# Optimization experiments

Measured on AMD Instinct MI355X. Metric: run time of the kernel, lower is better.

The kernel has to match this reference:

```python
import jax, jax.numpy as jnp
import numpy as np

B, L, D_IN, D, DEPTH, H = 1, 4095, 1536, 768, 4, 12
HD = D // H
FFN = 4 * D
GRID = 128
TILE = 256
SEGMENTS = (1024, 2048, 4096, 8192, 16384)
RATIOS = (1, 2, 4, 8, 16)
EPS = 1e-5
NEG = -1e9


def _sincos_1d(d, pos):
    omega = 1.0 / (10000.0 ** (np.arange(d // 2, dtype=np.float64) / (d / 2.0)))
    out = np.einsum('m,d->md', pos.reshape(-1).astype(np.float64), omega)
    return np.concatenate([np.sin(out), np.cos(out)], axis=1)


def _pos_embed_2d(d, g):
    # MAE-style 2d sincos grid; row index = coords[...,0], col = coords[...,1]
    gw, gh = np.meshgrid(np.arange(g, dtype=np.float64), np.arange(g, dtype=np.float64))
    emb_h = _sincos_1d(d // 2, gw)
    emb_w = _sincos_1d(d // 2, gh)
    pe = np.concatenate([emb_h, emb_w], axis=1)  # [g*g, d]
    return np.concatenate([np.zeros((1, d)), pe], axis=0).astype(np.float32)  # cls row


def setup_inputs() -> dict:
    key = jax.random.key(0)
    ks = jax.random.split(key, 16)
    n = lambda k, sh: 0.02 * jax.random.normal(k, sh, jnp.float32)
    x = jax.random.normal(ks[0], (B, L, D_IN), jnp.float32)
    coords = jax.random.uniform(ks[1], (B, L, 2), jnp.float32, 0.0, float(GRID * TILE))
    return {
        'x': x,
        'coords': coords,
        'pos_embed': jnp.asarray(_pos_embed_2d(D, GRID)),
        'cls_token': n(ks[2], (1, 1, D)),
        'patch_w': n(ks[3], (D_IN, D)),
        'patch_b': jnp.zeros((D,), jnp.float32),
        'ln1_g': jnp.ones((DEPTH, D), jnp.float32),
        'ln1_b': jnp.zeros((DEPTH, D), jnp.float32),
        'wq': n(ks[4], (DEPTH, D, D)), 'bq': jnp.zeros((DEPTH, D), jnp.float32),
        'wk': n(ks[5], (DEPTH, D, D)), 'bk': jnp.zeros((DEPTH, D), jnp.float32),
        'wv': n(ks[6], (DEPTH, D, D)), 'bv': jnp.zeros((DEPTH, D), jnp.float32),
        'wo': n(ks[7], (DEPTH, D, D)), 'bo': jnp.zeros((DEPTH, D), jnp.float32),
        'ln2_g': jnp.ones((DEPTH, D), jnp.float32),
        'ln2_b': jnp.zeros((DEPTH, D), jnp.float32),
        'w1': n(ks[8], (DEPTH, D, FFN)), 'b1': jnp.zeros((DEPTH, FFN), jnp.float32),
        'w2': n(ks[9], (DEPTH, FFN, D)), 'b2': jnp.zeros((DEPTH, D), jnp.float32),
        'enc_ln_g': jnp.ones((D,), jnp.float32),
        'enc_ln_b': jnp.zeros((D,), jnp.float32),
        'norm_g': jnp.ones((D,), jnp.float32),
        'norm_b': jnp.zeros((D,), jnp.float32),
    }


def _ln(t, g, b):
    m = t.mean(-1, keepdims=True)
    v = ((t - m) ** 2).mean(-1, keepdims=True)
    return (t - m) * jax.lax.rsqrt(v + EPS) * g + b


def _branch(q, k, v, w, r):
    # One LongNet dilated branch: segments of length w, per-head dilation r.
    Bq, S, Hh, hd = q.shape
    Lp = ((S + w - 1) // w) * w
    pad = Lp - S
    if pad:
        q = jnp.pad(q, ((0, 0), (0, pad), (0, 0), (0, 0)))
        k = jnp.pad(k, ((0, 0), (0, pad), (0, 0), (0, 0)))
        v = jnp.pad(v, ((0, 0), (0, pad), (0, 0), (0, 0)))
    n = Lp // w
    m = w // r
    # head-dependent offset subsampling (offset = head % r)
    idx = (jnp.arange(Hh) % r)[:, None] + r * jnp.arange(m)[None, :]  # [H, m]

    def seg(t):
        t = t.reshape(Bq, n, w, Hh, hd).transpose(0, 1, 3, 2, 4)  # [B,n,H,w,hd]
        return jnp.take_along_axis(t, idx[None, None, :, :, None], axis=3)  # [B,n,H,m,hd]

    qs, ks, vs = seg(q), seg(k), seg(v)
    valid = (jnp.arange(n)[:, None, None] * w + idx[None]) < S  # [n,H,m] key validity
    s = jnp.einsum('bnhqd,bnhkd->bnhqk', qs, ks)
    s = jnp.where(valid[None, :, :, None, :], s, NEG)
    lse_s = jax.scipy.special.logsumexp(s, axis=-1)              # [B,n,H,m]
    o_s = jnp.einsum('bnhqk,bnhkd->bnhqd', jax.nn.softmax(s, axis=-1), vs)
    hix = jnp.arange(Hh)[:, None]
    out = jnp.zeros((Bq, n, Hh, w, hd), q.dtype).at[:, :, hix, idx].set(o_s)
    lse = jnp.full((Bq, n, Hh, w), NEG, q.dtype).at[:, :, hix, idx].set(lse_s)
    out = out.transpose(0, 1, 3, 2, 4).reshape(Bq, Lp, Hh, hd)[:, :S]
    lse = lse.transpose(0, 1, 3, 2).reshape(Bq, Lp, Hh)[:, :S]
    return out, lse


def _forward(x, coords, pos_embed, cls_token, patch_w, patch_b, ln1_g, ln1_b,
             wq, bq, wk, bk, wv, bv, wo, bo, ln2_g, ln2_b, w1, b1, w2, b2,
             enc_ln_g, enc_ln_b, norm_g, norm_b):
    h = x @ patch_w + patch_b  # PatchEmbed (norm_layer=None -> Identity)
    c = jnp.floor(coords / TILE)
    pos = (c[..., 0] * GRID + c[..., 1]).astype(jnp.int32) + 1  # [B,L]
    h = h + pos_embed[pos]
    cls = jnp.broadcast_to(cls_token + pos_embed[0], (h.shape[0], 1, D))
    h = jnp.concatenate([cls, h], axis=1)  # [B, S, D], S = L+1
    S = h.shape[1]

    def layer(hcur, p):
        g1, bb1, wq_, bq_, wk_, bk_, wv_, bv_, wo_, bo_, g2, bb2, wf1, bf1, wf2, bf2 = p
        t = _ln(hcur, g1, bb1)
        q = (t @ wq_ + bq_).reshape(B, S, H, HD) * (HD ** -0.5)
        k = (t @ wk_ + bk_).reshape(B, S, H, HD)
        v = (t @ wv_ + bv_).reshape(B, S, H, HD)
        outs, lses = [], []
        for w_, r_ in zip(SEGMENTS, RATIOS):
            o, l = _branch(q, k, v, w_, r_)
            outs.append(o)
            lses.append(l)
        # LongNet combine: branches weighted by their softmax denominators
        wts = jax.nn.softmax(jnp.stack(lses), axis=0)  # [nb,B,S,H]
        attn = (wts[..., None] * jnp.stack(outs)).sum(0).reshape(B, S, D)
        hcur = hcur + attn @ wo_ + bo_
        t = _ln(hcur, g2, bb2)
        hcur = hcur + jax.nn.gelu(t @ wf1 + bf1) @ wf2 + bf2
        return hcur, None

    h, _ = jax.lax.scan(layer, h, (ln1_g, ln1_b, wq, bq, wk, bk, wv, bv,
                                   wo, bo, ln2_g, ln2_b, w1, b1, w2, b2))
    h = _ln(h, enc_ln_g, enc_ln_b)  # encoder final LN (normalize_before)
    h = _ln(h, norm_g, norm_b)      # module self.norm
    return h[:, 0]                  # cls token (global_pool=False)


def reference(x, coords, pos_embed, cls_token, patch_w, patch_b, ln1_g, ln1_b,
              wq, bq, wk, bk, wv, bv, wo, bo, ln2_g, ln2_b, w1, b1, w2, b2,
              enc_ln_g, enc_ln_b, norm_g, norm_b):
    return _forward(x, coords, pos_embed, cls_token, patch_w, patch_b, ln1_g, ln1_b,
                    wq, bq, wk, bk, wv, bv, wo, bo, ln2_g, ln2_b, w1, b1, w2, b2,
                    enc_ln_g, enc_ln_b, norm_g, norm_b)
```

## Files before the change

### kernel.cpp

```cpp
#include <hip/hip_runtime.h>
#include <hip/hip_bf16.h>
#include <math.h>
#include <stdint.h>

#define S_LEN 4096
#define L_LEN 4095
#define DIN   1536
#define DM    768
#define NHEAD 12
#define HDIM  64
#define FFND  3072
#define EPS   1e-5f

typedef unsigned short u16;
typedef unsigned int   u32;
typedef short short8 __attribute__((ext_vector_type(8)));
typedef float f32x4 __attribute__((ext_vector_type(4)));
typedef float f32x16 __attribute__((ext_vector_type(16)));
typedef int i32x2 __attribute__((ext_vector_type(2)));

__device__ __forceinline__ u16 f2b(float f) {
    union { float f; u32 u; } x; x.f = f;
    u32 r = (x.u + 0x7FFF + ((x.u >> 16) & 1)) >> 16;
    return (u16)r;
}
__device__ __forceinline__ float b2f(u16 v) {
    union { u32 u; float f; } x; x.u = ((u32)v) << 16;
    return x.f;
}
__device__ __forceinline__ float gelu_tanh(float x) {
    float x3 = x * x * x;
    return 0.5f * x * (1.f + tanhf(0.7978845608f * (x + 0.044715f * x3)));
}
__device__ __forceinline__ float block_reduce_sum(float v, float* sbuf) {
#pragma unroll
    for (int o = 32; o > 0; o >>= 1) v += __shfl_down(v, o, 64);
    __syncthreads();
    if ((threadIdx.x & 63) == 0) sbuf[threadIdx.x >> 6] = v;
    __syncthreads();
    return sbuf[0] + sbuf[1] + sbuf[2] + sbuf[3];
}
__device__ __forceinline__ void gload16(const void* g, void* l) {
    __builtin_amdgcn_global_load_lds((const __attribute__((address_space(1))) void*)g,
                                     (__attribute__((address_space(3))) void*)l,
                                     16, 0, 0);
}
__device__ __forceinline__ void lds_barrier() {
    asm volatile("s_waitcnt lgkmcnt(0)" ::: "memory");
    __builtin_amdgcn_s_barrier();
    __builtin_amdgcn_sched_barrier(0);
}

template <int BM, int BN>
__device__ __forceinline__ void gemm_bt(
    const u16* __restrict__ A, const u16* __restrict__ Bt,
    const float* __restrict__ bias, const float* __restrict__ res,
    float* __restrict__ outf, u16* __restrict__ outb,
    int M, int N, int K, float scale, int dogelu, int bx, int by)
{
    constexpr int MI = BM / 32;
    constexpr int NI = BN / 32;
    constexpr int AI = BM / 32;
    constexpr int BI = BN / 32;
    __shared__ u16 As[BM * 64];
    __shared__ u16 Bs[BN * 64];
    const int tid = threadIdx.x, wv = tid >> 6, l = tid & 63;
    const int bm = by * BM, bn = bx * BN;
    const int wm = wv >> 1, wn = wv & 1;

    f32x4 acc[MI][NI];
#pragma unroll
    for (int i = 0; i < MI; ++i)
#pragma unroll
        for (int j = 0; j < NI; ++j) acc[i][j] = (f32x4){0.f, 0.f, 0.f, 0.f};

    for (int k0 = 0; k0 < K; k0 += 64) {
#pragma unroll
        for (int i = 0; i < AI; ++i) {
            int row = (wv * AI + i) * 8 + (l >> 3);
            int col = ((l & 7) ^ (row & 7)) * 8;
            int grow = bm + row; if (grow > M - 1) grow = M - 1;
            gload16(A + (size_t)grow * K + k0 + col, &As[(wv * AI + i) * 512]);
        }
#pragma unroll
        for (int i = 0; i < BI; ++i) {
            int row = (wv * BI + i) * 8 + (l >> 3);
            int col = ((l & 7) ^ (row & 7)) * 8;
            gload16(Bt + (size_t)(bn + row) * K + k0 + col, &Bs[(wv * BI + i) * 512]);
        }
        __syncthreads();
#pragma unroll
        for (int kc = 0; kc < 2; ++kc) {
            short8 a[MI], b[NI];
#pragma unroll
            for (int mi = 0; mi < MI; ++mi) {
                int row = wm * (BM / 2) + mi * 16 + (l & 15);
                int off = ((l >> 4) * 16 + kc * 64) ^ ((row & 7) << 4);
                a[mi] = *(const short8*)&As[(row * 128 + off) >> 1];
            }
#pragma unroll
            for (int ni = 0; ni < NI; ++ni) {
                int row = wn * (BN / 2) + ni * 16 + (l & 15);
                int off = ((l >> 4) * 16 + kc * 64) ^ ((row & 7) << 4);
                b[ni] = *(const short8*)&Bs[(row * 128 + off) >> 1];
            }
#pragma unroll
            for (int mi = 0; mi < MI; ++mi)
#pragma unroll
                for (int ni = 0; ni < NI; ++ni)
                    acc[mi][ni] = __builtin_amdgcn_mfma_f32_16x16x32_bf16(
                        a[mi], b[ni], acc[mi][ni], 0, 0, 0);
        }
        __syncthreads();
    }
#pragma unroll
    for (int mi = 0; mi < MI; ++mi) {
#pragma unroll
        for (int rg = 0; rg < 4; ++rg) {
            int row = bm + wm * (BM / 2) + mi * 16 + (l >> 4) * 4 + rg;
            if (row >= M) continue;
#pragma unroll
            for (int ni = 0; ni < NI; ++ni) {
                int col = bn + wn * (BN / 2) + ni * 16 + (l & 15);
                float v = (acc[mi][ni][rg] + bias[col]) * scale;
                if (dogelu) v = gelu_tanh(v);
                if (res) v += res[(size_t)row * N + col];
                if (outf) outf[(size_t)row * N + col] = v;
                if (outb) outb[(size_t)row * N + col] = f2b(v);
            }
        }
    }
}

__global__ __launch_bounds__(256) void gemm128_kernel(
    const u16* __restrict__ A, const u16* __restrict__ Bt,
    const float* __restrict__ bias, const float* __restrict__ res,
    float* __restrict__ outf, u16* __restrict__ outb,
    int M, int N, int K, float scale, int dogelu)
{
    gemm_bt<128, 128>(A, Bt, bias, res, outf, outb, M, N, K, scale, dogelu,
                      blockIdx.x, blockIdx.y);
}
__global__ __launch_bounds__(256) void gemm12864_kernel(
    const u16* __restrict__ A, const u16* __restrict__ Bt,
    const float* __restrict__ bias, const float* __restrict__ res,
    float* __restrict__ outf, u16* __restrict__ outb,
    int M, int N, int K, float scale, int dogelu)
{
    gemm_bt<128, 64>(A, Bt, bias, res, outf, outb, M, N, K, scale, dogelu,
                     blockIdx.x, blockIdx.y);
}
__global__ __launch_bounds__(256) void qkv_kernel(
    const u16* __restrict__ t,
    const u16* __restrict__ wqT, const u16* __restrict__ wkT, const u16* __restrict__ wvT,
    const float* __restrict__ bq, const float* __restrict__ bk, const float* __restrict__ bv,
    u16* __restrict__ q, u16* __restrict__ k, u16* __restrict__ v)
{
    int z = blockIdx.z;
    const u16* B = (z == 0) ? wqT : (z == 1) ? wkT : wvT;
    const float* bias = (z == 0) ? bq : (z == 1) ? bk : bv;
    u16* C = (z == 0) ? q : (z == 1) ? k : v;
    float scale = (z == 0) ? 0.125f * 1.4426950408889634f : 1.0f;
    gemm_bt<128, 128>(t, B, bias, nullptr, nullptr, C, S_LEN, DM, DM, scale, 0,
                      blockIdx.x, blockIdx.y);
}

__global__ __launch_bounds__(256) void transpose_cvt(
    const float* __restrict__ s0, const float* __restrict__ s1,
    const float* __restrict__ s2, const float* __restrict__ s3,
    u16* __restrict__ dst, int K, int N)
{
    int z = blockIdx.z;
    const float* src = (z == 0) ? s0 : (z == 1) ? s1 : (z == 2) ? s2 : s3;
    u16* d = dst + (size_t)z * K * N;
    __shared__ float tile[64][65];
    const int t = threadIdx.x;
    const int tk = blockIdx.y * 64, tn = blockIdx.x * 64;
    const int r0 = t >> 4, c0 = (t & 15) * 4;
#pragma unroll
    for (int i = 0; i < 4; ++i) {
        const float* sp = &src[(size_t)(tk + r0 + i * 16) * N + tn + c0];
        tile[r0 + i * 16][c0 + 0] = sp[0];
        tile[r0 + i * 16][c0 + 1] = sp[1];
        tile[r0 + i * 16][c0 + 2] = sp[2];
        tile[r0 + i * 16][c0 + 3] = sp[3];
    }
    __syncthreads();
#pragma unroll
    for (int i = 0; i < 4; ++i) {
        int nr = r0 + i * 16;
        u32 lo = (u32)f2b(tile[c0 + 0][nr]) | ((u32)f2b(tile[c0 + 1][nr]) << 16);
        u32 hi = (u32)f2b(tile[c0 + 2][nr]) | ((u32)f2b(tile[c0 + 3][nr]) << 16);
        *(uint2*)&d[(size_t)(tn + nr) * K + tk + c0] = make_uint2(lo, hi);
    }
}

__global__ __launch_bounds__(256) void prep_weights(
    const float* __restrict__ wq, const float* __restrict__ wk,
    const float* __restrict__ wv, const float* __restrict__ wo,
    const float* __restrict__ w1, const float* __restrict__ w2,
    u16* __restrict__ wbase, int l0)
{
    const size_t DD = (size_t)DM * DM;
    const size_t DF = (size_t)DM * FFND;
    const int layer = l0 + blockIdx.y;
    const size_t lDD = (size_t)layer * DD;
    const size_t lDF = (size_t)layer * DF;
    u16* dstbase = wbase + (size_t)blockIdx.y * (4 * DD + 2 * DF);

    __shared__ float tile[64][65];
    const int id = blockIdx.x;
    const float* src; u16* dst; int K, N, tk64, tn64;
    if (id < 576) {
        int z = id / 144, rm = id % 144;
        src = ((z == 0) ? wq : (z == 1) ? wk : (z == 2) ? wv : wo) + lDD;
        dst = dstbase + (size_t)z * DD;
        K = DM; N = DM; tk64 = rm / 12; tn64 = rm % 12;
    } else if (id < 1152) {
        int rm = id - 576;
        src = w1 + lDF; dst = dstbase + 4 * DD;
        K = DM; N = FFND; tk64 = rm / 48; tn64 = rm % 48;
    } else {
        int rm = id - 1152;
        src = w2 + lDF; dst = dstbase + 4 * DD + DF;
        K = FFND; N = DM; tk64 = rm / 12; tn64 = rm % 12;
    }
    const int t = threadIdx.x;
    const int tk = tk64 * 64, tn = tn64 * 64;
    const int r0 = t >> 4, c0 = (t & 15) * 4;
#pragma unroll
    for (int i = 0; i < 4; ++i) {
        const float* sp = &src[(size_t)(tk + r0 + i * 16) * N + tn + c0];
        tile[r0 + i * 16][c0 + 0] = sp[0];
        tile[r0 + i * 16][c0 + 1] = sp[1];
        tile[r0 + i * 16][c0 + 2] = sp[2];
        tile[r0 + i * 16][c0 + 3] = sp[3];
    }
    __syncthreads();
#pragma unroll
    for (int i = 0; i < 4; ++i) {
        int nr = r0 + i * 16;
        u32 lo = (u32)f2b(tile[c0 + 0][nr]) | ((u32)f2b(tile[c0 + 1][nr]) << 16);
        u32 hi = (u32)f2b(tile[c0 + 2][nr]) | ((u32)f2b(tile[c0 + 3][nr]) << 16);
        *(uint2*)&dst[(size_t)(tn + nr) * K + tk + c0] = make_uint2(lo, hi);
    }
}

__global__ __launch_bounds__(256) void cvt_bf16_kernel(
    const float* __restrict__ x, u16* __restrict__ xb, int n4)
{
    int stride = gridDim.x * 256;
    for (int i = blockIdx.x * 256 + threadIdx.x; i < n4; i += stride) {
        float4 v = ((const float4*)x)[i];
        u32 lo = (u32)f2b(v.x) | ((u32)f2b(v.y) << 16);
        u32 hi = (u32)f2b(v.z) | ((u32)f2b(v.w) << 16);
        ((uint2*)xb)[i] = make_uint2(lo, hi);
    }
}

__global__ __launch_bounds__(192) void ln_kernel(
    const float* __restrict__ in, u16* __restrict__ out,
    const float* __restrict__ g, const float* __restrict__ b)
{
    __shared__ float sA[3], sB[3];
    const int s = blockIdx.x, tid = threadIdx.x;
    float4 x = ((const float4*)(in + (size_t)s * DM))[tid];
    float sum = x.x + x.y + x.z + x.w;
#pragma unroll
    for (int o = 32; o > 0; o >>= 1) sum += __shfl_down(sum, o, 64);
    if ((tid & 63) == 0) sA[tid >> 6] = sum;
    __syncthreads();
    float m = (sA[0] + sA[1] + sA[2]) * (1.f / DM);
    float dx = x.x - m, dy = x.y - m, dz = x.z - m, dw = x.w - m;
    float vs = dx * dx + dy * dy + dz * dz + dw * dw;
#pragma unroll
    for (int o = 32; o > 0; o >>= 1) vs += __shfl_down(vs, o, 64);
    if ((tid & 63) == 0) sB[tid >> 6] = vs;
    __syncthreads();
    float rs = rsqrtf((sB[0] + sB[1] + sB[2]) * (1.f / DM) + EPS);
    float4 gv = ((const float4*)g)[tid];
    float4 bv = ((const float4*)b)[tid];
    u32 lo = (u32)f2b(dx * rs * gv.x + bv.x) | ((u32)f2b(dy * rs * gv.y + bv.y) << 16);
    u32 hi = (u32)f2b(dz * rs * gv.z + bv.z) | ((u32)f2b(dw * rs * gv.w + bv.w) << 16);
    ((uint2*)(out + (size_t)s * DM))[tid] = make_uint2(lo, hi);
}

__global__ __launch_bounds__(256) void posadd_kernel(
    float* __restrict__ h, const float* __restrict__ coords,
    const float* __restrict__ pe, const float* __restrict__ cls)
{
    const int s = blockIdx.x;
    const int tid = threadIdx.x;
    if (s == 0) {
        for (int c = tid; c < DM; c += 256) h[c] = cls[c] + pe[c];
    } else {
        float c0 = floorf(coords[(size_t)(s - 1) * 2 + 0] * (1.f / 256.f));
        float c1 = floorf(coords[(size_t)(s - 1) * 2 + 1] * (1.f / 256.f));
        int pos = (int)(c0 * 128.f + c1) + 1;
        float* hr = h + (size_t)s * DM;
        const float* pr = pe + (size_t)pos * DM;
        for (int c = tid; c < DM; c += 256) hr[c] += pr[c];
    }
}

__global__ __launch_bounds__(256, 4) void attn_kernel(
    const u16* __restrict__ qb, const u16* __restrict__ kbuf, const u16* __restrict__ vb,
    u16* __restrict__ obuf, u16* __restrict__ tp, float* __restrict__ den)
{
    __shared__ u16 Vt[2][64 * 64];

    const int tid = threadIdx.x, wv = tid >> 6, l = tid & 63;
    const int lq = l & 31, lh = l >> 5;
    const int bid = blockIdx.x;
    int b, half = 0, qtile, head, seg = 0;
    if (bid < 768) {
        b = 0; int i = bid; half = i & 1; qtile = (i >> 1) & 7;
        int rest = i >> 4; head = rest % 12; seg = rest / 12;
    } else if (bid < 1152) {
        b = 1; int i = bid - 768; half = i & 1; qtile = (i >> 1) & 7;
        int rest = i >> 4; head = rest % 12; seg = rest / 12;
    } else if (bid < 1344) {
        b = 2; int i = bid - 1152; half = i & 1; qtile = (i >> 1) & 7;
        head = i >> 4;
    } else if (bid < 1392) {
        b = 3; int i = bid - 1344; qtile = i & 3; head = i >> 2;
    } else {
        b = 4; int i = bid - 1392; qtile = i & 1; head = i >> 1;
    }
    const int slot = (b < 3) ? b * 2 + half : 3 + b;
    const int r = 1 << b;
    const int w = 1024 << b;
    const int keyoff = (b < 3) ? half * 512 : 0;
    const int ntiles = (b == 4) ? 4 : 8;
    const size_t base = (size_t)seg * w + (head & (r - 1));
    const int q0 = qtile * 128 + wv * 32;
    const size_t kstep = (size_t)r * DM;

    const size_t sq_l = base + (size_t)r * (q0 + lq);
    const u16* qp = qb + sq_l * DM + head * 64 + lh * 8;
    short8 qf[4];
#pragma unroll
    for (int s = 0; s < 4; ++s) qf[s] = *(const short8*)(qp + s * 16);

    const u16* kp = kbuf + (base + (size_t)r * (keyoff + lq)) * DM + head * 64 + lh * 8;
    const int c = tid & 7, pp = tid >> 3;
    const u16* vsrc = vb + (base + (size_t)r * (keyoff + 2 * pp)) * DM + head * 64 + c * 8;

#define VPACK(dstbuf, A8, B8) do {                                          \
    _Pragma("unroll") for (int j = 0; j < 8; ++j) {                         \
        int i_ = (j + c) & 7; int hd_ = c * 8 + i_;                         \
        u32 val_ = (u32)(u16)(A8)[i_] | ((u32)(u16)(B8)[i_] << 16);         \
        int byte_ = hd_ * 128 + ((pp * 4) ^ (i_ << 4));                     \
        *(u32*)&Vt[dstbuf][byte_ >> 1] = val_; } } while (0)

    f32x16 oacc0 = {0.f,0.f,0.f,0.f,0.f,0.f,0.f,0.f,0.f,0.f,0.f,0.f,0.f,0.f,0.f,0.f};
    f32x16 oacc1 = oacc0;
    float dl = 0.f;

    short8 van = *(const short8*)vsrc;
    short8 vbn = *(const short8*)(vsrc + kstep);
    VPACK(0, van, vbn);
    van = *(const short8*)(vsrc + 64 * kstep);
    vbn = *(const short8*)(vsrc + 65 * kstep);
    short8 kf[8];
#pragma unroll
    for (int s = 0; s < 4; ++s) {
        kf[s]     = *(const short8*)(kp + s * 16);
        kf[4 + s] = *(const short8*)(kp + 32 * kstep + s * 16);
    }
    lds_barrier();

    for (int t = 0; t < ntiles; ++t) {
        const int curb = t & 1;
        f32x16 s0 = {0.f,0.f,0.f,0.f,0.f,0.f,0.f,0.f,0.f,0.f,0.f,0.f,0.f,0.f,0.f,0.f};
        f32x16 s1 = s0;
#pragma unroll
        for (int s = 0; s < 4; ++s)
            s0 = __builtin_amdgcn_mfma_f32_32x32x16_bf16(kf[s], qf[s], s0, 0, 0, 0);
#pragma unroll
        for (int s = 0; s < 4; ++s)
            s1 = __builtin_amdgcn_mfma_f32_32x32x16_bf16(kf[4 + s], qf[s], s1, 0, 0, 0);

        if (t + 1 < ntiles) {
            const u16* kn = kp + (size_t)(t + 1) * 64 * kstep;
#pragma unroll
            for (int s = 0; s < 4; ++s) {
                kf[s]     = *(const short8*)(kn + s * 16);
                kf[4 + s] = *(const short8*)(kn + 32 * kstep + s * 16);
            }
        }

        float ds = 0.f;
#pragma unroll
        for (int i = 0; i < 16; ++i) { s0[i] = exp2f(s0[i]); ds += s0[i]; }
#pragma unroll
        for (int i = 0; i < 16; ++i) { s1[i] = exp2f(s1[i]); ds += s1[i]; }
        ds += __shfl_xor(ds, 32, 64);
        dl += ds;

        if (t + 1 < ntiles) VPACK(curb ^ 1, van, vbn);
        if (t + 2 < ntiles) {
            van = *(const short8*)(vsrc + (size_t)(t + 2) * 64 * kstep);
            vbn = *(const short8*)(vsrc + ((size_t)(t + 2) * 64 + 1) * kstep);
        }

#pragma unroll
        for (int kb2 = 0; kb2 < 2; ++kb2) {
            u32 wd[8];
#pragma unroll
            for (int j = 0; j < 8; ++j) {
                float lo = (kb2 == 0) ? s0[2 * j] : s1[2 * j];
                float hi = (kb2 == 0) ? s0[2 * j + 1] : s1[2 * j + 1];
                asm("v_cvt_pk_bf16_f32 %0, %1, %2" : "=v"(wd[j]) : "v"(lo), "v"(hi));
            }
#pragma unroll
            for (int ks2 = 0; ks2 < 2; ++ks2) {
                i32x2 X = __builtin_amdgcn_permlane32_swap(
                    (int)wd[ks2 * 4 + 0], (int)wd[ks2 * 4 + 2], false, false);
                i32x2 Y = __builtin_amdgcn_permlane32_swap(
                    (int)wd[ks2 * 4 + 1], (int)wd[ks2 * 4 + 3], false, false);
                union { u32 u[4]; short8 s; } pk;
                pk.u[0] = (u32)X[0]; pk.u[1] = (u32)Y[0];
                pk.u[2] = (u32)X[1]; pk.u[3] = (u32)Y[1];
                const int tt = kb2 * 2 + ks2;
#pragma unroll
                for (int hg = 0; hg < 2; ++hg) {
                    int row = hg * 32 + lq;
                    int byteoff = row * 128 + ((lh * 16 + tt * 32) ^ ((row & 7) << 4));
                    short8 vf = *(const short8*)&Vt[curb][byteoff >> 1];
                    if (hg == 0)
                        oacc0 = __builtin_amdgcn_mfma_f32_32x32x16_bf16(pk.s, vf, oacc0, 0, 0, 0);
                    else
                        oacc1 = __builtin_amdgcn_mfma_f32_32x32x16_bf16(pk.s, vf, oacc1, 0, 0, 0);
                }
            }
        }
        lds_barrier();
    }

    u16* ob = (slot == 7) ? tp : obuf + (size_t)slot * S_LEN * DM;
    float* den_b = den + (size_t)slot * S_LEN * NHEAD;
    if (l < 32) den_b[sq_l * NHEAD + head] = dl;
#pragma unroll
    for (int reg = 0; reg < 16; ++reg) {
        int qloc = (reg & 3) + 8 * (reg >> 2) + 4 * lh;
        size_t sq = base + (size_t)r * (q0 + qloc);
        u16* orow = ob + sq * DM + head * 64;
        u32 pk2;
        asm("v_cvt_pk_bf16_f32 %0, %1, %2"
            : "=v"(pk2) : "v"(oacc0[reg]), "v"(oacc1[reg]));
        orow[lq]      = (u16)(pk2 & 0xffff);
        orow[32 + lq] = (u16)(pk2 >> 16);
    }
#undef VPACK
}

__global__ __launch_bounds__(192) void combine_kernel(
    const u16* __restrict__ obuf, const float* __restrict__ den,
    u16* __restrict__ t)
{
    const int s = blockIdx.x;
    const int tid = threadIdx.x;
    const int c0 = tid * 4, head = c0 >> 6;
    const size_t SD = (size_t)S_LEN * DM;
    const size_t SN = (size_t)S_LEN * NHEAD;
    const int sx = s ^ head;
    bool val[8];
    val[0] = val[1] = true;
    val[2] = val[3] = (sx & 1) == 0;
    val[4] = val[5] = (sx & 3) == 0;
    val[6] = (sx & 7) == 0;
    val[7] = (s & 15) == head;
    float wsum = 0.f, o0 = 0.f, o1 = 0.f, o2 = 0.f, o3 = 0.f;
#pragma unroll
    for (int b = 0; b < 8; ++b) {
        if (val[b]) {
            wsum += den[b * SN + (size_t)s * NHEAD + head];
            const u16* src = (b == 7) ? t : obuf + (size_t)b * SD;
            uint2 u = *(const uint2*)(src + (size_t)s * DM + c0);
            o0 += b2f((u16)(u.x & 0xffff));
            o1 += b2f((u16)(u.x >> 16));
            o2 += b2f((u16)(u.y & 0xffff));
            o3 += b2f((u16)(u.y >> 16));
        }
    }
    float inv = 1.f / wsum;
    u32 lo = (u32)f2b(o0 * inv) | ((u32)f2b(o1 * inv) << 16);
    u32 hi = (u32)f2b(o2 * inv) | ((u32)f2b(o3 * inv) << 16);
    ((uint2*)(t + (size_t)s * DM))[tid] = make_uint2(lo, hi);
}

__global__ __launch_bounds__(256) void cls_attn_kernel(
    const u16* __restrict__ qb, const u16* __restrict__ kb,
    const u16* __restrict__ vb, float* __restrict__ cpart,
    float* __restrict__ lsep)
{
    __shared__ float q0[64];
    __shared__ float pbuf[128];
    __shared__ float red[8];
    __shared__ float po[256];
    const int blk = blockIdx.x, tid = threadIdx.x;
    int b, head, chunk;
    if (blk < 96)       { b = 0; head = blk >> 3; chunk = blk & 7; }
    else if (blk < 144) { int i = blk - 96;  b = 1; head = (i >> 3) * 2; chunk = i & 7; }
    else if (blk < 168) { int i = blk - 144; b = 2; head = (i >> 3) * 4; chunk = i & 7; }
    else if (blk < 176) { int i = blk - 168; b = 3; head = (i >> 2) * 8; chunk = i & 3; }
    else                { int i = blk - 176; b = 4; head = 0;            chunk = i; }
    const int r = 1 << b;
    if (tid < 64) q0[tid] = b2f(qb[head * 64 + tid]);
    __syncthreads();

    float sc = -1e30f;
    if (tid < 128) {
        const int j = chunk * 128 + tid;
        const u16* kp = kb + (size_t)j * r * DM + head * 64;
        float acc = 0.f;
#pragma unroll
        for (int d8 = 0; d8 < 8; ++d8) {
            short8 kv = *(const short8*)(kp + d8 * 8);
#pragma unroll
            for (int jj = 0; jj < 8; ++jj)
                acc += q0[d8 * 8 + jj] * b2f((u16)kv[jj]);
        }
        sc = acc;
    }
    float mxw = sc;
#pragma unroll
    for (int o = 1; o < 64; o <<= 1) mxw = fmaxf(mxw, __shfl_xor(mxw, o, 64));
    if ((tid & 63) == 0) red[tid >> 6] = mxw;
    __syncthreads();
    const float bm = fmaxf(red[0], red[1]);
    float p = 0.f;
    if (tid < 128) { p = exp2f(sc - bm); pbuf[tid] = p; }
    float sw = p;
#pragma unroll
    for (int o = 1; o < 64; o <<= 1) sw += __shfl_xor(sw, o, 64);
    if ((tid & 63) == 0) red[4 + (tid >> 6)] = sw;
    __syncthreads();
    const float dsum = red[4] + red[5];

    const int hd = tid & 63, ch = tid >> 6;
    const u16* vp = vb + (size_t)(chunk * 128 + ch * 32) * r * DM + head * 64 + hd;
    const size_t vstep = (size_t)r * DM;
    float o = 0.f;
#pragma unroll 8
    for (int j = 0; j < 32; ++j)
        o += pbuf[ch * 32 + j] * b2f(vp[(size_t)j * vstep]);
    po[tid] = o;
    __syncthreads();
    if (tid < 64)
        cpart[(size_t)blk * 64 + tid] =
            (po[tid] + po[tid + 64] + po[tid + 128] + po[tid + 192]) / dsum;
    if (tid == 0) lsep[blk] = bm + log2f(dsum);
}

__global__ __launch_bounds__(64) void cls_combine_kernel(
    const float* __restrict__ cpart, const float* __restrict__ lsep,
    u16* __restrict__ t)
{
    const int head = blockIdx.x, tid = threadIdx.x;
#define FORALL_PARTS(EXPR)                                                    \
    for (int c = 0; c < 8; ++c) { int blk = head * 8 + c; EXPR; }             \
    if (!(head & 1)) for (int c = 0; c < 8; ++c) { int blk = 96 + (head >> 1) * 8 + c; EXPR; } \
    if (!(head & 3)) for (int c = 0; c < 8; ++c) { int blk = 144 + (head >> 2) * 8 + c; EXPR; } \
    if (!(head & 7)) for (int c = 0; c < 4; ++c) { int blk = 168 + (head >> 3) * 4 + c; EXPR; } \
    if (head == 0)  for (int c = 0; c < 2; ++c) { int blk = 176 + c; EXPR; }
    float mx = -1e30f;
    FORALL_PARTS(mx = fmaxf(mx, lsep[blk]))
    float ws = 0.f, ov = 0.f;
    FORALL_PARTS({ float wb = exp2f(lsep[blk] - mx); ws += wb;
                   ov += wb * cpart[(size_t)blk * 64 + tid]; })
    t[head * 64 + tid] = f2b(ov / ws);
#undef FORALL_PARTS
}

__global__ __launch_bounds__(256) void row_gemv_kernel(
    const u16* __restrict__ x, const u16* __restrict__ wT,
    const float* __restrict__ bias, const float* __restrict__ res,
    float* __restrict__ outf, u16* __restrict__ outb, int K, int dogelu)
{
    __shared__ float xs[3072];
    const int tid = threadIdx.x;
    for (int i = tid; i < K; i += 256) xs[i] = b2f(x[i]);
    __syncthreads();
    const int n = blockIdx.x * 32 + (tid >> 3);
    const int kp = tid & 7;
    const u16* wrow = wT + (size_t)n * K;
    float acc = 0.f;
    for (int k = kp * 8; k < K; k += 64) {
        short8 wv = *(const short8*)(wrow + k);
#pragma unroll
        for (int j = 0; j < 8; ++j) acc += xs[k + j] * b2f((u16)wv[j]);
    }
    acc += __shfl_down(acc, 4, 8);
    acc += __shfl_down(acc, 2, 8);
    acc += __shfl_down(acc, 1, 8);
    if (kp == 0) {
        float v = acc + bias[n];
        if (dogelu) v = gelu_tanh(v);
        if (res) v += res[n];
        if (outf) outf[n] = v;
        if (outb) outb[n] = f2b(v);
    }
}

__global__ __launch_bounds__(256) void final_ln_kernel(
    const float* __restrict__ h,
    const float* __restrict__ g1, const float* __restrict__ b1,
    const float* __restrict__ g2, const float* __restrict__ b2,
    float* __restrict__ out)
{
    __shared__ float sbuf[4];
    const int tid = threadIdx.x;
    float x0 = h[tid], x1 = h[tid + 256], x2 = h[tid + 512];
    float m = block_reduce_sum(x0 + x1 + x2, sbuf) * (1.f / DM);
    float d0 = x0 - m, d1 = x1 - m, d2 = x2 - m;
    float var = block_reduce_sum(d0 * d0 + d1 * d1 + d2 * d2, sbuf) * (1.f / DM);
    float rs = rsqrtf(var + EPS);
    float y0 = d0 * rs * g1[tid]       + b1[tid];
    float y1 = d1 * rs * g1[tid + 256] + b1[tid + 256];
    float y2 = d2 * rs * g1[tid + 512] + b1[tid + 512];
    m = block_reduce_sum(y0 + y1 + y2, sbuf) * (1.f / DM);
    d0 = y0 - m; d1 = y1 - m; d2 = y2 - m;
    var = block_reduce_sum(d0 * d0 + d1 * d1 + d2 * d2, sbuf) * (1.f / DM);
    rs = rsqrtf(var + EPS);
    out[tid]       = d0 * rs * g2[tid]       + b2[tid];
    out[tid + 256] = d1 * rs * g2[tid + 256] + b2[tid + 256];
    out[tid + 512] = d2 * rs * g2[tid + 512] + b2[tid + 512];
}

extern "C" void kernel_launch(void* const* d_in, const int* in_sizes, int n_in,
                              void* d_out, int out_size, void* d_ws, size_t ws_size,
                              hipStream_t stream)
{
    (void)in_sizes; (void)n_in; (void)out_size;
    const float* x        = (const float*)d_in[0];
    const float* coords   = (const float*)d_in[1];
    const float* pos_emb  = (const float*)d_in[2];
    const float* cls_tok  = (const float*)d_in[3];
    const float* patch_w  = (const float*)d_in[4];
    const float* patch_b  = (const float*)d_in[5];
    const float* ln1_g    = (const float*)d_in[6];
    const float* ln1_b    = (const float*)d_in[7];
    const float* wq       = (const float*)d_in[8];
    const float* bq       = (const float*)d_in[9];
    const float* wk       = (const float*)d_in[10];
    const float* bk       = (const float*)d_in[11];
    const float* wv       = (const float*)d_in[12];
    const float* bv       = (const float*)d_in[13];
    const float* wo       = (const float*)d_in[14];
    const float* bo       = (const float*)d_in[15];
    const float* ln2_g    = (const float*)d_in[16];
    const float* ln2_b    = (const float*)d_in[17];
    const float* w1       = (const float*)d_in[18];
    const float* b1       = (const float*)d_in[19];
    const float* w2       = (const float*)d_in[20];
    const float* b2       = (const float*)d_in[21];
    const float* enc_g    = (const float*)d_in[22];
    const float* enc_b    = (const float*)d_in[23];
    const float* norm_g   = (const float*)d_in[24];
    const float* norm_b   = (const float*)d_in[25];
    float* out = (float*)d_out;

    const size_t SD = (size_t)S_LEN * DM;
    const size_t DD = (size_t)DM * DM;
    const size_t DF = (size_t)DM * FFND;
    const size_t SN = (size_t)S_LEN * NHEAD;
    const size_t WSTRIDE = 4 * DD + 2 * DF;

    char* p = (char*)d_ws;
    float* h   = (float*)p;              p += SD * 4;
    u16* t     = (u16*)p;                p += SD * 2;
    u16* qb    = (u16*)p;                p += SD * 2;
    u16* kb    = (u16*)p;                p += SD * 2;
    u16* vb    = (u16*)p;                p += SD * 2;
    float* den = (float*)p;              p += 8 * SN * 4;
    u16* obuf  = (u16*)p;                p += 7 * SD * 2;
    u16* ffn   = obuf;
    u16* xb    = obuf;
    u16* pwT   = (u16*)p;                p += (size_t)DIN * DM * 2;
    u16* wbase = (u16*)p;
    const size_t used_base = (size_t)(p - (char*)d_ws);
    const bool all4 = ws_size >= used_base + 4 * WSTRIDE * 2;
    float* cpart = den;
    float* lsep  = den + 178 * 64;

    cvt_bf16_kernel<<<2048, 256, 0, stream>>>(x, xb, (L_LEN * DIN) / 4);
    transpose_cvt<<<dim3(DM / 64, DIN / 64, 1), 256, 0, stream>>>(
        patch_w, patch_w, patch_w, patch_w, pwT, DIN, DM);
    gemm12864_kernel<<<dim3(12, 32), 256, 0, stream>>>(
        xb, pwT, patch_b, nullptr, h + DM, nullptr, L_LEN, DM, DIN, 1.f, 0);
    posadd_kernel<<<S_LEN, 256, 0, stream>>>(h, coords, pos_emb, cls_tok);

    if (all4)
        prep_weights<<<dim3(1728, 4), 256, 0, stream>>>(
            wq, wk, wv, wo, w1, w2, wbase, 0);

    for (int l = 0; l < 4; ++l) {
        if (!all4)
            prep_weights<<<dim3(1728, 1), 256, 0, stream>>>(
                wq, wk, wv, wo, w1, w2, wbase, l);
        u16* wT  = wbase + (all4 ? (size_t)l * WSTRIDE : 0);
        u16* w1T = wT + 4 * DD;
        u16* w2T = w1T + DF;

        ln_kernel<<<S_LEN, 192, 0, stream>>>(h, t, ln1_g + l * DM, ln1_b + l * DM);
        qkv_kernel<<<dim3(6, 32, 3), 256, 0, stream>>>(
            t, wT, wT + DD, wT + 2 * DD,
            bq + l * DM, bk + l * DM, bv + l * DM, qb, kb, vb);

        if (l < 3) {
            attn_kernel<<<1416, 256, 0, stream>>>(qb, kb, vb, obuf, t, den);
            combine_kernel<<<S_LEN, 192, 0, stream>>>(obuf, den, t);
            gemm12864_kernel<<<dim3(12, 32), 256, 0, stream>>>(
                t, wT + 3 * DD, bo + l * DM, h, h, nullptr, S_LEN, DM, DM, 1.f, 0);
            ln_kernel<<<S_LEN, 192, 0, stream>>>(h, t, ln2_g + l * DM, ln2_b + l * DM);
            gemm128_kernel<<<dim3(24, 32), 256, 0, stream>>>(
                t, w1T, b1 + (size_t)l * FFND, nullptr, nullptr, ffn,
                S_LEN, FFND, DM, 1.f, 1);
            gemm12864_kernel<<<dim3(12, 32), 256, 0, stream>>>(
                ffn, w2T, b2 + l * DM, h, h, nullptr, S_LEN, DM, FFND, 1.f, 0);
        } else {
            cls_attn_kernel<<<178, 256, 0, stream>>>(qb, kb, vb, cpart, lsep);
            cls_combine_kernel<<<NHEAD, 64, 0, stream>>>(cpart, lsep, t);
            row_gemv_kernel<<<24, 256, 0, stream>>>(
                t, wT + 3 * DD, bo + l * DM, h, h, nullptr, DM, 0);
            ln_kernel<<<1, 192, 0, stream>>>(h, t, ln2_g + l * DM, ln2_b + l * DM);
            row_gemv_kernel<<<96, 256, 0, stream>>>(
                t, w1T, b1 + (size_t)l * FFND, nullptr, nullptr, ffn, DM, 1);
            row_gemv_kernel<<<24, 256, 0, stream>>>(
                ffn, w2T, b2 + l * DM, h, h, nullptr, FFND, 0);
        }
    }
    final_ln_kernel<<<1, 256, 0, stream>>>(h, enc_g, enc_b, norm_g, norm_b, out);
}
```

Baseline: 1.069 ms.

## Use 64x64 GEMM tiles, swizzle attention block order, prep weights per layer

Replaces the 128x64 GEMM tile with 64x64 for the patch-embed, out-projection and FFN2 GEMMs, doubling the grid to 768 blocks so more CUs are busy on N=768 outputs. Attention blocks are remapped with an 8-way interleave so heavy and light segment branches spread across XCDs. Weight conversion now runs per layer into a single reused buffer instead of converting all four layers upfront. This removes the workspace-size branch but puts a conversion launch inside each layer. Smaller tiles lower data reuse per block.

```diff
diff --git a/kernel.cpp b/kernel.cpp
--- a/kernel.cpp
+++ b/kernel.cpp
@@ -141,14 +141,14 @@
     gemm_bt<128, 128>(A, Bt, bias, res, outf, outb, M, N, K, scale, dogelu,
                       blockIdx.x, blockIdx.y);
 }
-__global__ __launch_bounds__(256) void gemm12864_kernel(
+__global__ __launch_bounds__(256) void gemm6464_kernel(
     const u16* __restrict__ A, const u16* __restrict__ Bt,
     const float* __restrict__ bias, const float* __restrict__ res,
     float* __restrict__ outf, u16* __restrict__ outb,
     int M, int N, int K, float scale, int dogelu)
 {
-    gemm_bt<128, 64>(A, Bt, bias, res, outf, outb, M, N, K, scale, dogelu,
-                     blockIdx.x, blockIdx.y);
+    gemm_bt<64, 64>(A, Bt, bias, res, outf, outb, M, N, K, scale, dogelu,
+                    blockIdx.x, blockIdx.y);
 }
 __global__ __launch_bounds__(256) void qkv_kernel(
     const u16* __restrict__ t,
@@ -199,31 +199,22 @@
     const float* __restrict__ wq, const float* __restrict__ wk,
     const float* __restrict__ wv, const float* __restrict__ wo,
     const float* __restrict__ w1, const float* __restrict__ w2,
-    u16* __restrict__ wbase, int l0)
-{
-    const size_t DD = (size_t)DM * DM;
-    const size_t DF = (size_t)DM * FFND;
-    const int layer = l0 + blockIdx.y;
-    const size_t lDD = (size_t)layer * DD;
-    const size_t lDF = (size_t)layer * DF;
-    u16* dstbase = wbase + (size_t)blockIdx.y * (4 * DD + 2 * DF);
-
+    u16* __restrict__ wTdd, u16* __restrict__ w1T, u16* __restrict__ w2T)
+{
     __shared__ float tile[64][65];
     const int id = blockIdx.x;
     const float* src; u16* dst; int K, N, tk64, tn64;
     if (id < 576) {
         int z = id / 144, rm = id % 144;
-        src = ((z == 0) ? wq : (z == 1) ? wk : (z == 2) ? wv : wo) + lDD;
-        dst = dstbase + (size_t)z * DD;
+        src = (z == 0) ? wq : (z == 1) ? wk : (z == 2) ? wv : wo;
+        dst = wTdd + (size_t)z * DM * DM;
         K = DM; N = DM; tk64 = rm / 12; tn64 = rm % 12;
     } else if (id < 1152) {
         int rm = id - 576;
-        src = w1 + lDF; dst = dstbase + 4 * DD;
-        K = DM; N = FFND; tk64 = rm / 48; tn64 = rm % 48;
+        src = w1; dst = w1T; K = DM; N = FFND; tk64 = rm / 48; tn64 = rm % 48;
     } else {
         int rm = id - 1152;
-        src = w2 + lDF; dst = dstbase + 4 * DD + DF;
-        K = FFND; N = DM; tk64 = rm / 12; tn64 = rm % 12;
+        src = w2; dst = w2T; K = FFND; N = DM; tk64 = rm / 12; tn64 = rm % 12;
     }
     const int t = threadIdx.x;
     const int tk = tk64 * 64, tn = tn64 * 64;
@@ -311,7 +302,7 @@
 
     const int tid = threadIdx.x, wv = tid >> 6, l = tid & 63;
     const int lq = l & 31, lh = l >> 5;
-    const int bid = blockIdx.x;
+    const int bid = (blockIdx.x & 7) * 177 + (blockIdx.x >> 3);
     int b, half = 0, qtile, head, seg = 0;
     if (bid < 768) {
         b = 0; int i = bid; half = i & 1; qtile = (i >> 1) & 7;
@@ -633,7 +624,7 @@
                               void* d_out, int out_size, void* d_ws, size_t ws_size,
                               hipStream_t stream)
 {
-    (void)in_sizes; (void)n_in; (void)out_size;
+    (void)in_sizes; (void)n_in; (void)out_size; (void)ws_size;
     const float* x        = (const float*)d_in[0];
     const float* coords   = (const float*)d_in[1];
     const float* pos_emb  = (const float*)d_in[2];
@@ -666,7 +657,6 @@
     const size_t DD = (size_t)DM * DM;
     const size_t DF = (size_t)DM * FFND;
     const size_t SN = (size_t)S_LEN * NHEAD;
-    const size_t WSTRIDE = 4 * DD + 2 * DF;
 
     char* p = (char*)d_ws;
     float* h   = (float*)p;              p += SD * 4;
@@ -679,52 +669,47 @@
     u16* ffn   = obuf;
     u16* xb    = obuf;
     u16* pwT   = (u16*)p;                p += (size_t)DIN * DM * 2;
-    u16* wbase = (u16*)p;
-    const size_t used_base = (size_t)(p - (char*)d_ws);
-    const bool all4 = ws_size >= used_base + 4 * WSTRIDE * 2;
+    u16* wTdd  = (u16*)p;                p += 4 * DD * 2;
+    u16* w1T   = (u16*)p;                p += DF * 2;
+    u16* w2T   = (u16*)p;                p += DF * 2;
     float* cpart = den;
     float* lsep  = den + 178 * 64;
 
     cvt_bf16_kernel<<<2048, 256, 0, stream>>>(x, xb, (L_LEN * DIN) / 4);
     transpose_cvt<<<dim3(DM / 64, DIN / 64, 1), 256, 0, stream>>>(
         patch_w, patch_w, patch_w, patch_w, pwT, DIN, DM);
-    gemm12864_kernel<<<dim3(12, 32), 256, 0, stream>>>(
+    gemm6464_kernel<<<dim3(DM / 64, 64), 256, 0, stream>>>(
         xb, pwT, patch_b, nullptr, h + DM, nullptr, L_LEN, DM, DIN, 1.f, 0);
     posadd_kernel<<<S_LEN, 256, 0, stream>>>(h, coords, pos_emb, cls_tok);
 
-    if (all4)
-        prep_weights<<<dim3(1728, 4), 256, 0, stream>>>(
-            wq, wk, wv, wo, w1, w2, wbase, 0);
-
     for (int l = 0; l < 4; ++l) {
-        if (!all4)
-            prep_weights<<<dim3(1728, 1), 256, 0, stream>>>(
-                wq, wk, wv, wo, w1, w2, wbase, l);
-        u16* wT  = wbase + (all4 ? (size_t)l * WSTRIDE : 0);
-        u16* w1T = wT + 4 * DD;
-        u16* w2T = w1T + DF;
+        const size_t lDD = (size_t)l * DD;
+        const size_t lDF = (size_t)l * DF;
+        prep_weights<<<1728, 256, 0, stream>>>(
+            wq + lDD, wk + lDD, wv + lDD, wo + lDD, w1 + lDF, w2 + lDF,
+            wTdd, w1T, w2T);
 
         ln_kernel<<<S_LEN, 192, 0, stream>>>(h, t, ln1_g + l * DM, ln1_b + l * DM);
         qkv_kernel<<<dim3(6, 32, 3), 256, 0, stream>>>(
-            t, wT, wT + DD, wT + 2 * DD,
+            t, wTdd, wTdd + DD, wTdd + 2 * DD,
             bq + l * DM, bk + l * DM, bv + l * DM, qb, kb, vb);
 
         if (l < 3) {
             attn_kernel<<<1416, 256, 0, stream>>>(qb, kb, vb, obuf, t, den);
             combine_kernel<<<S_LEN, 192, 0, stream>>>(obuf, den, t);
-            gemm12864_kernel<<<dim3(12, 32), 256, 0, stream>>>(
-                t, wT + 3 * DD, bo + l * DM, h, h, nullptr, S_LEN, DM, DM, 1.f, 0);
+            gemm6464_kernel<<<dim3(12, 64), 256, 0, stream>>>(
+                t, wTdd + 3 * DD, bo + l * DM, h, h, nullptr, S_LEN, DM, DM, 1.f, 0);
             ln_kernel<<<S_LEN, 192, 0, stream>>>(h, t, ln2_g + l * DM, ln2_b + l * DM);
             gemm128_kernel<<<dim3(24, 32), 256, 0, stream>>>(
                 t, w1T, b1 + (size_t)l * FFND, nullptr, nullptr, ffn,
                 S_LEN, FFND, DM, 1.f, 1);
-            gemm12864_kernel<<<dim3(12, 32), 256, 0, stream>>>(
+            gemm6464_kernel<<<dim3(12, 64), 256, 0, stream>>>(
                 ffn, w2T, b2 + l * DM, h, h, nullptr, S_LEN, DM, FFND, 1.f, 0);
         } else {
             cls_attn_kernel<<<178, 256, 0, stream>>>(qb, kb, vb, cpart, lsep);
             cls_combine_kernel<<<NHEAD, 64, 0, stream>>>(cpart, lsep, t);
             row_gemv_kernel<<<24, 256, 0, stream>>>(
-                t, wT + 3 * DD, bo + l * DM, h, h, nullptr, DM, 0);
+                t, wTdd + 3 * DD, bo + l * DM, h, h, nullptr, DM, 0);
             ln_kernel<<<1, 192, 0, stream>>>(h, t, ln2_g + l * DM, ln2_b + l * DM);
             row_gemv_kernel<<<96, 256, 0, stream>>>(
                 t, w1T, b1 + (size_t)l * FFND, nullptr, nullptr, ffn, DM, 1);
```

Result: faster. 968.6 us (median of 2 runs) (-9.4%).
